# Optimization experiments

Hardware: AMD Instinct MI355X
Metric: run time of the kernel (lower is better)

The kernel has to match this reference:

```python
import jax, jax.numpy as jnp
import numpy as np

B = 4096          # events
L = 524288        # total set points (avg 128 per event)
CIN = 16          # per-point feature size (set feature 'a')
DVEC = 32         # flat feature size (feature 'b')
PHI = [128, 128, 64]
MLP = [256, 128]
EPS = 1e-5        # BatchNorm1d eps


def setup_inputs() -> dict:
    key = jax.random.key(0)
    ks = jax.random.split(key, 10)
    def n(k, shape, scale=0.05):
        return jax.random.normal(k, shape, dtype=jnp.float32) * scale
    return {
        "x_a": jax.random.normal(ks[0], (1, CIN, L), dtype=jnp.float32),
        "x_b": jax.random.normal(ks[1], (B, DVEC), dtype=jnp.float32),
        # row 0 -> counts for set feature 'a'; row 1 ignored (Reshape branch)
        "sample_indices": jnp.full((2, B), L // B, dtype=jnp.int32),
        "W1": n(ks[2], (PHI[0], CIN)),  "b1": jnp.zeros((PHI[0],), jnp.float32),
        "W2": n(ks[3], (PHI[1], PHI[0])), "b2": jnp.zeros((PHI[1],), jnp.float32),
        "W3": n(ks[4], (PHI[2], PHI[1])), "b3": jnp.zeros((PHI[2],), jnp.float32),
        "Wm1": n(ks[5], (MLP[0], PHI[2] + DVEC)), "bm1": jnp.zeros((MLP[0],), jnp.float32),
        "g1": jnp.ones((MLP[0],), jnp.float32), "be1": jnp.zeros((MLP[0],), jnp.float32),
        "Wm2": n(ks[6], (MLP[1], MLP[0])), "bm2": jnp.zeros((MLP[1],), jnp.float32),
        "g2": jnp.ones((MLP[1],), jnp.float32), "be2": jnp.zeros((MLP[1],), jnp.float32),
        "Wm3": n(ks[7], (1, MLP[1])), "bm3": jnp.zeros((1,), jnp.float32),
    }


def _bn(x, g, b):
    # BatchNorm1d, training-mode batch stats, biased variance (torch semantics)
    mu = jnp.mean(x, axis=0)
    var = jnp.var(x, axis=0)
    return (x - mu) * jax.lax.rsqrt(var + EPS) * g + b


def reference(x_a, x_b, sample_indices,
              W1, b1, W2, b2, W3, b3,
              Wm1, bm1, g1, be1, Wm2, bm2, g2, be2, Wm3, bm3):
    counts = sample_indices[0].astype(jnp.int32)                       # [B]
    bounds = jnp.concatenate([jnp.zeros((1,), jnp.int32), jnp.cumsum(counts)])  # [B+1]

    # PhiNet: pointwise Conv1d stack (kernel size 1) on [CIN, L]
    h = x_a[0]
    h = jax.nn.relu(jnp.einsum('oc,cl->ol', W1, h) + b1[:, None])
    h = jax.nn.relu(jnp.einsum('oc,cl->ol', W2, h) + b2[:, None])
    h = jax.nn.relu(jnp.einsum('oc,cl->ol', W3, h) + b3[:, None])      # [64, L]

    # fused segment-mean: point p belongs to segment j iff bounds[j] <= p < bounds[j+1]
    seg = jnp.searchsorted(bounds, jnp.arange(h.shape[1], dtype=jnp.int32), side='right') - 1
    sums = jax.ops.segment_sum(h.T, seg, num_segments=counts.shape[0])  # [B, 64]
    means = sums / jnp.maximum(counts, 1).astype(jnp.float32)[:, None]

    # feature order: sorted keys -> ('a' set repr, 'b' flat)
    z = jnp.concatenate([means, x_b.reshape(-1, DVEC)], axis=1)        # [B, 96]

    z = jax.nn.relu(_bn(z @ Wm1.T + bm1, g1, be1))
    z = jax.nn.relu(_bn(z @ Wm2.T + bm2, g2, be2))
    return jax.nn.sigmoid(z @ Wm3.T + bm3)                             # [B, 1]
```

## Files before the change

### kernel.cpp

```cpp
#include <hip/hip_runtime.h>
#include <hip/hip_bf16.h>

#define B_EVENTS 4096
#define L_PTS    524288
#define CIN      16
#define C1       128
#define C2       128
#define C3       64
#define DVEC     32
#define ZDIM     96
#define M1       256
#define M2       128
#define BN_EPS   1e-5f
#define TPTS     32
#define EPB      2

typedef __attribute__((ext_vector_type(8))) short bf16x8;
typedef __attribute__((ext_vector_type(4))) float f32x4;

__device__ __forceinline__ ushort f2bf(float x) {
    union { float f; unsigned u; } a; a.f = x;
    unsigned r = (a.u + 0x7fffu + ((a.u >> 16) & 1u)) >> 16;
    return (ushort)r;
}

__device__ __forceinline__ unsigned cvtpk(float lo, float hi) {
    unsigned r;
    asm("v_cvt_pk_bf16_f32 %0, %1, %2" : "=v"(r) : "v"(lo), "v"(hi));
    return r;
}

__device__ __forceinline__ unsigned long long pack4relu(f32x4 a) {
    union { unsigned u[2]; unsigned long long ll; } pk;
    pk.u[0] = cvtpk(fmaxf(a[0], 0.f), fmaxf(a[1], 0.f));
    pk.u[1] = cvtpk(fmaxf(a[2], 0.f), fmaxf(a[3], 0.f));
    return pk.ll;
}

__device__ __forceinline__ int ldsoff(int base, int rowSlots, int c, int sir) {
    int s = c * rowSlots + sir;
    s ^= (c & 7);
    return base + s * 16;
}

__global__ __launch_bounds__(1024) void scanprep_kernel(
    const int* __restrict__ si, int* __restrict__ bounds, float* __restrict__ stats,
    const float* __restrict__ W1, const float* __restrict__ W2, const float* __restrict__ W3,
    ushort* __restrict__ w1p, ushort* __restrict__ w2b, ushort* __restrict__ w3b)
{
    if (blockIdx.x == 0) {
        __shared__ int sh[1024];
        const int tid = threadIdx.x;
        const int c0 = si[tid*4+0], c1 = si[tid*4+1], c2 = si[tid*4+2], c3 = si[tid*4+3];
        const int s4 = c0 + c1 + c2 + c3;
        sh[tid] = s4;
        if (tid < 768) stats[tid] = 0.f;
        __syncthreads();
        for (int off = 1; off < 1024; off <<= 1) {
            int add = (tid >= off) ? sh[tid - off] : 0;
            __syncthreads();
            sh[tid] += add;
            __syncthreads();
        }
        const int excl = (tid == 0) ? 0 : sh[tid - 1];
        bounds[tid*4+0] = excl;
        bounds[tid*4+1] = excl + c0;
        bounds[tid*4+2] = excl + c0 + c1;
        bounds[tid*4+3] = excl + c0 + c1 + c2;
        if (tid == 1023) bounds[B_EVENTS] = excl + s4;
    } else {
        const int tid = (blockIdx.x - 1) * 1024 + threadIdx.x;
        const int nthr = 4 * 1024;
        for (int i = tid; i < C1 * 32; i += nthr) {
            const int r = i >> 5, k = i & 31;
            w1p[i] = (k < CIN) ? f2bf(W1[r * CIN + k]) : (ushort)0;
        }
        for (int i = tid; i < C2 * C1; i += nthr) w2b[i] = f2bf(W2[i]);
        for (int i = tid; i < C3 * C2; i += nthr) w3b[i] = f2bf(W3[i]);
    }
}

__global__ __launch_bounds__(128, 2) void phi_mfma_kernel(
    const float* __restrict__ xa, const float* __restrict__ xb,
    const int* __restrict__ bounds,
    const ushort* __restrict__ w1p, const ushort* __restrict__ w2b, const ushort* __restrict__ w3b,
    const float* __restrict__ b1, const float* __restrict__ b2, const float* __restrict__ b3,
    float* __restrict__ z)
{
    __shared__ __align__(16) char lds[18432];
    __shared__ float msum[C3];

    const int tid  = threadIdx.x;
    const int lane = tid & 63;
    const int wm   = tid >> 6;
    const int g4   = lane >> 4;
    const int c16  = lane & 15;

    bf16x8 a1[4], a2[4][4], a3[2][4];
    {
        const int r1 = wm * 64 + c16;
        #pragma unroll
        for (int mf = 0; mf < 4; ++mf)
            a1[mf] = *(const bf16x8*)&w1p[(r1 + mf * 16) * 32 + g4 * 8];
        #pragma unroll
        for (int mf = 0; mf < 4; ++mf)
            #pragma unroll
            for (int kf = 0; kf < 4; ++kf)
                a2[mf][kf] = *(const bf16x8*)&w2b[(r1 + mf * 16) * C1 + kf * 32 + g4 * 8];
        const int r3 = wm * 32 + c16;
        #pragma unroll
        for (int mf = 0; mf < 2; ++mf)
            #pragma unroll
            for (int kf = 0; kf < 4; ++kf)
                a3[mf][kf] = *(const bf16x8*)&w3b[(r3 + mf * 16) * C2 + kf * 32 + g4 * 8];
    }

    const int pt   = tid & 31;
    const int qrt  = tid >> 5;
    const int xoff = ldsoff(0, 4, pt, qrt >> 1) + (qrt & 1) * 8;

    for (int e = 0; e < EPB; ++e) {
        const int j     = blockIdx.x * EPB + e;
        const int start = bounds[j];
        const int cnt   = bounds[j + 1] - start;

        if (tid < C3) msum[tid] = 0.f;

        float xr[4];
        #pragma unroll
        for (int jj = 0; jj < 4; ++jj)
            xr[jj] = (pt < cnt) ? xa[(size_t)(qrt * 4 + jj) * L_PTS + start + pt] : 0.f;
        {
            union { unsigned u[2]; unsigned long long ll; } pk;
            pk.u[0] = cvtpk(xr[0], xr[1]);
            pk.u[1] = cvtpk(xr[2], xr[3]);
            *(unsigned long long*)(lds + xoff) = pk.ll;
        }
        __syncthreads();

        for (int p0 = 0; p0 < cnt; p0 += TPTS) {
            const bool more = (p0 + TPTS) < cnt;

            if (more) {
                const int p = p0 + TPTS + pt;
                #pragma unroll
                for (int jj = 0; jj < 4; ++jj)
                    xr[jj] = (p < cnt) ? xa[(size_t)(qrt * 4 + jj) * L_PTS + start + p] : 0.f;
            }

            {
                f32x4 acc[4][2];
                #pragma unroll
                for (int mf = 0; mf < 4; ++mf) {
                    const f32x4 bb = *(const f32x4*)&b1[wm * 64 + mf * 16 + g4 * 4];
                    acc[mf][0] = bb; acc[mf][1] = bb;
                }
                bf16x8 bfrag[2];
                #pragma unroll
                for (int nf = 0; nf < 2; ++nf)
                    bfrag[nf] = *(const bf16x8*)(lds + ldsoff(0, 4, nf * 16 + c16, g4));
                __builtin_amdgcn_s_setprio(1);
                #pragma unroll
                for (int nf = 0; nf < 2; ++nf)
                    #pragma unroll
                    for (int mf = 0; mf < 4; ++mf)
                        acc[mf][nf] = __builtin_amdgcn_mfma_f32_16x16x32_bf16(a1[mf], bfrag[nf], acc[mf][nf], 0, 0, 0);
                __builtin_amdgcn_s_setprio(0);
                #pragma unroll
                for (int mf = 0; mf < 4; ++mf)
                    #pragma unroll
                    for (int nf = 0; nf < 2; ++nf) {
                        const int c = nf * 16 + c16;
                        const int sir = (wm * 64 + mf * 16) / 8 + (g4 >> 1);
                        *(unsigned long long*)(lds + ldsoff(2048, 16, c, sir) + (g4 & 1) * 8) = pack4relu(acc[mf][nf]);
                    }
            }
            __syncthreads();

            {
                f32x4 acc[4][2];
                #pragma unroll
                for (int mf = 0; mf < 4; ++mf) {
                    const f32x4 bb = *(const f32x4*)&b2[wm * 64 + mf * 16 + g4 * 4];
                    acc[mf][0] = bb; acc[mf][1] = bb;
                }
                #pragma unroll
                for (int nf = 0; nf < 2; ++nf) {
                    const int c = nf * 16 + c16;
                    bf16x8 bk[4];
                    #pragma unroll
                    for (int kf = 0; kf < 4; ++kf)
                        bk[kf] = *(const bf16x8*)(lds + ldsoff(2048, 16, c, kf * 4 + g4));
                    __builtin_amdgcn_s_setprio(1);
                    #pragma unroll
                    for (int mf = 0; mf < 4; ++mf)
                        #pragma unroll
                        for (int kf = 0; kf < 4; ++kf)
                            acc[mf][nf] = __builtin_amdgcn_mfma_f32_16x16x32_bf16(a2[mf][kf], bk[kf], acc[mf][nf], 0, 0, 0);
                    __builtin_amdgcn_s_setprio(0);
                }
                #pragma unroll
                for (int mf = 0; mf < 4; ++mf)
                    #pragma unroll
                    for (int nf = 0; nf < 2; ++nf) {
                        const int c = nf * 16 + c16;
                        const int sir = (wm * 64 + mf * 16) / 8 + (g4 >> 1);
                        *(unsigned long long*)(lds + ldsoff(10240, 16, c, sir) + (g4 & 1) * 8) = pack4relu(acc[mf][nf]);
                    }
            }
            __syncthreads();

            if (more) {
                union { unsigned u[2]; unsigned long long ll; } pk;
                pk.u[0] = cvtpk(xr[0], xr[1]);
                pk.u[1] = cvtpk(xr[2], xr[3]);
                *(unsigned long long*)(lds + xoff) = pk.ll;
            }

            {
                f32x4 acc3[2][2];
                #pragma unroll
                for (int mf = 0; mf < 2; ++mf) {
                    const f32x4 bb = *(const f32x4*)&b3[wm * 32 + mf * 16 + g4 * 4];
                    acc3[mf][0] = bb; acc3[mf][1] = bb;
                }
                #pragma unroll
                for (int nf = 0; nf < 2; ++nf) {
                    const int c = nf * 16 + c16;
                    bf16x8 bk[4];
                    #pragma unroll
                    for (int kf = 0; kf < 4; ++kf)
                        bk[kf] = *(const bf16x8*)(lds + ldsoff(10240, 16, c, kf * 4 + g4));
                    __builtin_amdgcn_s_setprio(1);
                    #pragma unroll
                    for (int mf = 0; mf < 2; ++mf)
                        #pragma unroll
                        for (int kf = 0; kf < 4; ++kf)
                            acc3[mf][nf] = __builtin_amdgcn_mfma_f32_16x16x32_bf16(a3[mf][kf], bk[kf], acc3[mf][nf], 0, 0, 0);
                    __builtin_amdgcn_s_setprio(0);
                }
                float s[2][4];
                #pragma unroll
                for (int mf = 0; mf < 2; ++mf)
                    #pragma unroll
                    for (int r = 0; r < 4; ++r) s[mf][r] = 0.f;
                #pragma unroll
                for (int nf = 0; nf < 2; ++nf) {
                    const int col = p0 + nf * 16 + c16;
                    const bool valid = col < cnt;
                    #pragma unroll
                    for (int mf = 0; mf < 2; ++mf)
                        #pragma unroll
                        for (int r = 0; r < 4; ++r) {
                            const float v = fmaxf(acc3[mf][nf][r], 0.f);
                            if (valid) s[mf][r] += v;
                        }
                }
                #pragma unroll
                for (int mf = 0; mf < 2; ++mf)
                    #pragma unroll
                    for (int r = 0; r < 4; ++r) {
                        float v = s[mf][r];
                        #pragma unroll
                        for (int m = 1; m < 16; m <<= 1) v += __shfl_xor(v, m, 64);
                        s[mf][r] = v;
                    }
                if (c16 == 0) {
                    #pragma unroll
                    for (int mf = 0; mf < 2; ++mf)
                        #pragma unroll
                        for (int r = 0; r < 4; ++r)
                            atomicAdd(&msum[wm * 32 + mf * 16 + g4 * 4 + r], s[mf][r]);
                }
            }
            __syncthreads();
        }

        if (tid < C3) {
            const float inv = 1.f / (float)max(cnt, 1);
            z[(size_t)j * ZDIM + tid] = msum[tid] * inv;
        } else if (tid < ZDIM) {
            z[(size_t)j * ZDIM + tid] = xb[(size_t)j * DVEC + (tid - C3)];
        }
    }
}

__global__ __launch_bounds__(256) void mlp1_kernel(
    const float* __restrict__ z, const float* __restrict__ Wm1, const float* __restrict__ bm1,
    float* __restrict__ y1, float* __restrict__ gsum, float* __restrict__ gsq)
{
    __shared__ float zs[8][ZDIM + 4];
    const int r0 = blockIdx.x * 8;
    const int tid = threadIdx.x;
    for (int i = tid; i < 8 * ZDIM; i += 256) {
        const int r = i / ZDIM, c = i - r * ZDIM;
        zs[r][c] = z[(size_t)(r0 + r) * ZDIM + c];
    }
    __syncthreads();
    const int o = tid;
    float acc[8];
    const float bb = bm1[o];
    #pragma unroll
    for (int r = 0; r < 8; ++r) acc[r] = bb;
    for (int c = 0; c < ZDIM; c += 4) {
        const float4 w = *(const float4*)&Wm1[o * ZDIM + c];
        #pragma unroll
        for (int r = 0; r < 8; ++r) {
            const float4 v = *(const float4*)&zs[r][c];
            acc[r] += w.x*v.x + w.y*v.y + w.z*v.z + w.w*v.w;
        }
    }
    float s = 0.f, sq = 0.f;
    #pragma unroll
    for (int r = 0; r < 8; ++r) {
        y1[(size_t)(r0 + r) * M1 + o] = acc[r];
        s += acc[r]; sq += acc[r] * acc[r];
    }
    atomicAdd(&gsum[o], s);
    atomicAdd(&gsq[o], sq);
}

__global__ void bnfin_kernel(const float* __restrict__ gsum, const float* __restrict__ gsq,
                             const float* __restrict__ g, const float* __restrict__ be,
                             float* __restrict__ scale, float* __restrict__ shift, int n)
{
    const int o = blockIdx.x * blockDim.x + threadIdx.x;
    if (o >= n) return;
    const float mu  = gsum[o] * (1.f / B_EVENTS);
    const float var = gsq[o] * (1.f / B_EVENTS) - mu * mu;
    const float rs  = rsqrtf(var + BN_EPS);
    const float sc  = rs * g[o];
    scale[o] = sc;
    shift[o] = be[o] - mu * sc;
}

__global__ __launch_bounds__(256) void mlp2_kernel(
    const float* __restrict__ y1, const float* __restrict__ scale1, const float* __restrict__ shift1,
    const float* __restrict__ Wm2, const float* __restrict__ bm2,
    float* __restrict__ y2, float* __restrict__ gsum, float* __restrict__ gsq)
{
    __shared__ float zs[8][M1 + 4];
    const int r0 = blockIdx.x * 8;
    const int tid = threadIdx.x;
    for (int i = tid; i < 8 * M1; i += 256) {
        const int r = i >> 8, c = i & (M1 - 1);
        const float v = y1[(size_t)(r0 + r) * M1 + c];
        zs[r][c] = fmaxf(v * scale1[c] + shift1[c], 0.f);
    }
    __syncthreads();
    const int o = tid & 127;
    const int h = tid >> 7;
    float acc[4];
    const float bb = bm2[o];
    #pragma unroll
    for (int r = 0; r < 4; ++r) acc[r] = bb;
    for (int c = 0; c < M1; c += 4) {
        const float4 w = *(const float4*)&Wm2[o * M1 + c];
        #pragma unroll
        for (int r = 0; r < 4; ++r) {
            const float4 v = *(const float4*)&zs[h * 4 + r][c];
            acc[r] += w.x*v.x + w.y*v.y + w.z*v.z + w.w*v.w;
        }
    }
    float s = 0.f, sq = 0.f;
    #pragma unroll
    for (int r = 0; r < 4; ++r) {
        y2[(size_t)(r0 + h * 4 + r) * M2 + o] = acc[r];
        s += acc[r]; sq += acc[r] * acc[r];
    }
    atomicAdd(&gsum[o], s);
    atomicAdd(&gsq[o], sq);
}

__global__ __launch_bounds__(256) void final_kernel(
    const float* __restrict__ y2, const float* __restrict__ scale2, const float* __restrict__ shift2,
    const float* __restrict__ Wm3, const float* __restrict__ bm3,
    float* __restrict__ out)
{
    const int tid = threadIdx.x;
    const int w = tid >> 6, l = tid & 63;
    const int r = blockIdx.x * 4 + w;
    const float e0 = fmaxf(y2[(size_t)r * M2 + l]      * scale2[l]      + shift2[l],      0.f);
    const float e1 = fmaxf(y2[(size_t)r * M2 + 64 + l] * scale2[64 + l] + shift2[64 + l], 0.f);
    float a = e0 * Wm3[l] + e1 * Wm3[64 + l];
    #pragma unroll
    for (int off = 32; off >= 1; off >>= 1) a += __shfl_down(a, off, 64);
    if (l == 0) out[r] = 1.f / (1.f + expf(-(a + bm3[0])));
}

extern "C" void kernel_launch(void* const* d_in, const int* in_sizes, int n_in,
                              void* d_out, int out_size, void* d_ws, size_t ws_size,
                              hipStream_t stream) {
    const float* xa  = (const float*)d_in[0];
    const float* xb  = (const float*)d_in[1];
    const int*   si  = (const int*)  d_in[2];
    const float* W1  = (const float*)d_in[3];
    const float* b1  = (const float*)d_in[4];
    const float* W2  = (const float*)d_in[5];
    const float* b2  = (const float*)d_in[6];
    const float* W3  = (const float*)d_in[7];
    const float* b3  = (const float*)d_in[8];
    const float* Wm1 = (const float*)d_in[9];
    const float* bm1 = (const float*)d_in[10];
    const float* g1  = (const float*)d_in[11];
    const float* be1 = (const float*)d_in[12];
    const float* Wm2 = (const float*)d_in[13];
    const float* bm2 = (const float*)d_in[14];
    const float* g2  = (const float*)d_in[15];
    const float* be2 = (const float*)d_in[16];
    const float* Wm3 = (const float*)d_in[17];
    const float* bm3 = (const float*)d_in[18];
    float* out = (float*)d_out;

    char* ws = (char*)d_ws;
    size_t off = 0;
    auto alloc = [&](size_t bytes) -> void* {
        void* p = ws + off;
        off = (off + bytes + 255) & ~(size_t)255;
        return p;
    };
    int*    bounds = (int*)   alloc((B_EVENTS + 1) * sizeof(int));
    float*  stats  = (float*) alloc(768 * sizeof(float));
    float*  z      = (float*) alloc((size_t)B_EVENTS * ZDIM * sizeof(float));
    float*  y1     = (float*) alloc((size_t)B_EVENTS * M1 * sizeof(float));
    float*  y2     = (float*) alloc((size_t)B_EVENTS * M2 * sizeof(float));
    float*  scale1 = (float*) alloc(M1 * sizeof(float));
    float*  shift1 = (float*) alloc(M1 * sizeof(float));
    float*  scale2 = (float*) alloc(M2 * sizeof(float));
    float*  shift2 = (float*) alloc(M2 * sizeof(float));
    ushort* w1p    = (ushort*)alloc(C1 * 32 * sizeof(ushort));
    ushort* w2b    = (ushort*)alloc(C2 * C1 * sizeof(ushort));
    ushort* w3b    = (ushort*)alloc(C3 * C2 * sizeof(ushort));
    float* gsum1 = stats;
    float* gsq1  = stats + 256;
    float* gsum2 = stats + 512;
    float* gsq2  = stats + 640;

    hipLaunchKernelGGL(scanprep_kernel, dim3(5), dim3(1024), 0, stream,
                       si, bounds, stats, W1, W2, W3, w1p, w2b, w3b);
    hipLaunchKernelGGL(phi_mfma_kernel, dim3(B_EVENTS / EPB), dim3(128), 0, stream,
                       xa, xb, bounds, w1p, w2b, w3b, b1, b2, b3, z);
    hipLaunchKernelGGL(mlp1_kernel, dim3(B_EVENTS / 8), dim3(256), 0, stream,
                       z, Wm1, bm1, y1, gsum1, gsq1);
    hipLaunchKernelGGL(bnfin_kernel, dim3(1), dim3(256), 0, stream,
                       gsum1, gsq1, g1, be1, scale1, shift1, M1);
    hipLaunchKernelGGL(mlp2_kernel, dim3(B_EVENTS / 8), dim3(256), 0, stream,
                       y1, scale1, shift1, Wm2, bm2, y2, gsum2, gsq2);
    hipLaunchKernelGGL(bnfin_kernel, dim3(1), dim3(128), 0, stream,
                       gsum2, gsq2, g2, be2, scale2, shift2, M2);
    hipLaunchKernelGGL(final_kernel, dim3(B_EVENTS / 4), dim3(256), 0, stream,
                       y2, scale2, shift2, Wm3, bm3, out);
}
```

Before: 146.9 us.

## Double phi tile to 64 points with 4 waves, prefetch across events, fold BN finalize

The phi kernel now runs 256 threads over 64-point tiles, with waves split along the point dimension. It prefetches the next event's inputs during the current event's last tile, and keeps the segment sums in registers, reducing them once per event instead of using per-tile LDS atomics and a barrier. The two single-block bnfin kernels are removed, and their scale/shift computation is folded into the prologues of mlp2 and final, which cuts two launches. LDS use per block roughly doubles, which may reduce occupancy.

```diff
diff --git a/kernel.cpp b/kernel.cpp
--- a/kernel.cpp
+++ b/kernel.cpp
@@ -12,7 +12,7 @@
 #define M1       256
 #define M2       128
 #define BN_EPS   1e-5f
-#define TPTS     32
+#define TPTS     64
 #define EPB      2
 
 typedef __attribute__((ext_vector_type(8))) short bf16x8;
@@ -80,19 +80,20 @@
     }
 }
 
-__global__ __launch_bounds__(128, 2) void phi_mfma_kernel(
+__global__ __launch_bounds__(256, 2) void phi_mfma_kernel(
     const float* __restrict__ xa, const float* __restrict__ xb,
     const int* __restrict__ bounds,
     const ushort* __restrict__ w1p, const ushort* __restrict__ w2b, const ushort* __restrict__ w3b,
     const float* __restrict__ b1, const float* __restrict__ b2, const float* __restrict__ b3,
     float* __restrict__ z)
 {
-    __shared__ __align__(16) char lds[18432];
-    __shared__ float msum[C3];
+    __shared__ __align__(16) char lds[37376];
 
     const int tid  = threadIdx.x;
     const int lane = tid & 63;
-    const int wm   = tid >> 6;
+    const int wid  = tid >> 6;
+    const int wm   = wid >> 1;
+    const int wn   = wid & 1;
     const int g4   = lane >> 4;
     const int c16  = lane & 15;
 
@@ -115,37 +116,54 @@
                 a3[mf][kf] = *(const bf16x8*)&w3b[(r3 + mf * 16) * C2 + kf * 32 + g4 * 8];
     }
 
-    const int pt   = tid & 31;
-    const int qrt  = tid >> 5;
-    const int xoff = ldsoff(0, 4, pt, qrt >> 1) + (qrt & 1) * 8;
-
-    for (int e = 0; e < EPB; ++e) {
-        const int j     = blockIdx.x * EPB + e;
-        const int start = bounds[j];
-        const int cnt   = bounds[j + 1] - start;
-
-        if (tid < C3) msum[tid] = 0.f;
-
-        float xr[4];
-        #pragma unroll
-        for (int jj = 0; jj < 4; ++jj)
-            xr[jj] = (pt < cnt) ? xa[(size_t)(qrt * 4 + jj) * L_PTS + start + pt] : 0.f;
-        {
+    const int pt = tid & 63;
+    const int q  = tid >> 6;
+    const int xw = pt * 32 + q * 8;
+
+    if (tid < 128)
+        *(unsigned long long*)(lds + (tid >> 1) * 32 + 16 + (tid & 1) * 8) = 0ull;
+
+    int j     = blockIdx.x * EPB;
+    int start = bounds[j];
+    int end   = bounds[j + 1];
+    int cnt   = end - start;
+    bool staged = false;
+
+    for (int e = 0; e < EPB; ++e, ++j) {
+        int end2 = 0, cnt2 = 0;
+        if (e + 1 < EPB) { end2 = bounds[j + 2]; cnt2 = end2 - end; }
+
+        if (!staged) {
             union { unsigned u[2]; unsigned long long ll; } pk;
-            pk.u[0] = cvtpk(xr[0], xr[1]);
-            pk.u[1] = cvtpk(xr[2], xr[3]);
-            *(unsigned long long*)(lds + xoff) = pk.ll;
-        }
-        __syncthreads();
+            float v0 = (pt < cnt) ? xa[(size_t)(q * 4 + 0) * L_PTS + start + pt] : 0.f;
+            float v1 = (pt < cnt) ? xa[(size_t)(q * 4 + 1) * L_PTS + start + pt] : 0.f;
+            float v2 = (pt < cnt) ? xa[(size_t)(q * 4 + 2) * L_PTS + start + pt] : 0.f;
+            float v3 = (pt < cnt) ? xa[(size_t)(q * 4 + 3) * L_PTS + start + pt] : 0.f;
+            pk.u[0] = cvtpk(v0, v1);
+            pk.u[1] = cvtpk(v2, v3);
+            *(unsigned long long*)(lds + xw) = pk.ll;
+            __syncthreads();
+        }
+
+        float s[2][4];
+        #pragma unroll
+        for (int mf = 0; mf < 2; ++mf)
+            #pragma unroll
+            for (int r = 0; r < 4; ++r) s[mf][r] = 0.f;
 
         for (int p0 = 0; p0 < cnt; p0 += TPTS) {
-            const bool more = (p0 + TPTS) < cnt;
-
-            if (more) {
-                const int p = p0 + TPTS + pt;
-                #pragma unroll
-                for (int jj = 0; jj < 4; ++jj)
-                    xr[jj] = (p < cnt) ? xa[(size_t)(qrt * 4 + jj) * L_PTS + start + p] : 0.f;
+            const bool inEvt  = (p0 + TPTS) < cnt;
+            const bool nxtEvt = !inEvt && (e + 1 < EPB);
+            const bool pre    = inEvt || nxtEvt;
+
+            float xr0 = 0.f, xr1 = 0.f, xr2 = 0.f, xr3 = 0.f;
+            if (pre) {
+                const int nbase = inEvt ? (start + p0 + TPTS) : end;
+                const int nrem  = inEvt ? (cnt - p0 - TPTS) : cnt2;
+                xr0 = (pt < nrem) ? xa[(size_t)(q * 4 + 0) * L_PTS + nbase + pt] : 0.f;
+                xr1 = (pt < nrem) ? xa[(size_t)(q * 4 + 1) * L_PTS + nbase + pt] : 0.f;
+                xr2 = (pt < nrem) ? xa[(size_t)(q * 4 + 2) * L_PTS + nbase + pt] : 0.f;
+                xr3 = (pt < nrem) ? xa[(size_t)(q * 4 + 3) * L_PTS + nbase + pt] : 0.f;
             }
 
             {
@@ -158,7 +176,7 @@
                 bf16x8 bfrag[2];
                 #pragma unroll
                 for (int nf = 0; nf < 2; ++nf)
-                    bfrag[nf] = *(const bf16x8*)(lds + ldsoff(0, 4, nf * 16 + c16, g4));
+                    bfrag[nf] = *(const bf16x8*)(lds + (wn * 32 + nf * 16 + c16) * 32 + g4 * 16);
                 __builtin_amdgcn_s_setprio(1);
                 #pragma unroll
                 for (int nf = 0; nf < 2; ++nf)
@@ -170,9 +188,9 @@
                 for (int mf = 0; mf < 4; ++mf)
                     #pragma unroll
                     for (int nf = 0; nf < 2; ++nf) {
-                        const int c = nf * 16 + c16;
+                        const int c = wn * 32 + nf * 16 + c16;
                         const int sir = (wm * 64 + mf * 16) / 8 + (g4 >> 1);
-                        *(unsigned long long*)(lds + ldsoff(2048, 16, c, sir) + (g4 & 1) * 8) = pack4relu(acc[mf][nf]);
+                        *(unsigned long long*)(lds + ldsoff(4096, 16, c, sir) + (g4 & 1) * 8) = pack4relu(acc[mf][nf]);
                     }
             }
             __syncthreads();
@@ -186,11 +204,11 @@
                 }
                 #pragma unroll
                 for (int nf = 0; nf < 2; ++nf) {
-                    const int c = nf * 16 + c16;
+                    const int c = wn * 32 + nf * 16 + c16;
                     bf16x8 bk[4];
                     #pragma unroll
                     for (int kf = 0; kf < 4; ++kf)
-                        bk[kf] = *(const bf16x8*)(lds + ldsoff(2048, 16, c, kf * 4 + g4));
+                        bk[kf] = *(const bf16x8*)(lds + ldsoff(4096, 16, c, kf * 4 + g4));
                     __builtin_amdgcn_s_setprio(1);
                     #pragma unroll
                     for (int mf = 0; mf < 4; ++mf)
@@ -199,23 +217,22 @@
                             acc[mf][nf] = __builtin_amdgcn_mfma_f32_16x16x32_bf16(a2[mf][kf], bk[kf], acc[mf][nf], 0, 0, 0);
                     __builtin_amdgcn_s_setprio(0);
                 }
+                if (pre) {
+                    union { unsigned u[2]; unsigned long long ll; } pk;
+                    pk.u[0] = cvtpk(xr0, xr1);
+                    pk.u[1] = cvtpk(xr2, xr3);
+                    *(unsigned long long*)(lds + xw) = pk.ll;
+                }
                 #pragma unroll
                 for (int mf = 0; mf < 4; ++mf)
                     #pragma unroll
                     for (int nf = 0; nf < 2; ++nf) {
-                        const int c = nf * 16 + c16;
+                        const int c = wn * 32 + nf * 16 + c16;
                         const int sir = (wm * 64 + mf * 16) / 8 + (g4 >> 1);
-                        *(unsigned long long*)(lds + ldsoff(10240, 16, c, sir) + (g4 & 1) * 8) = pack4relu(acc[mf][nf]);
+                        *(unsigned long long*)(lds + ldsoff(20480, 16, c, sir) + (g4 & 1) * 8) = pack4relu(acc[mf][nf]);
                     }
             }
             __syncthreads();
-
-            if (more) {
-                union { unsigned u[2]; unsigned long long ll; } pk;
-                pk.u[0] = cvtpk(xr[0], xr[1]);
-                pk.u[1] = cvtpk(xr[2], xr[3]);
-                *(unsigned long long*)(lds + xoff) = pk.ll;
-            }
 
             {
                 f32x4 acc3[2][2];
@@ -226,11 +243,11 @@
                 }
                 #pragma unroll
                 for (int nf = 0; nf < 2; ++nf) {
-                    const int c = nf * 16 + c16;
+                    const int c = wn * 32 + nf * 16 + c16;
                     bf16x8 bk[4];
                     #pragma unroll
                     for (int kf = 0; kf < 4; ++kf)
-                        bk[kf] = *(const bf16x8*)(lds + ldsoff(10240, 16, c, kf * 4 + g4));
+                        bk[kf] = *(const bf16x8*)(lds + ldsoff(20480, 16, c, kf * 4 + g4));
                     __builtin_amdgcn_s_setprio(1);
                     #pragma unroll
                     for (int mf = 0; mf < 2; ++mf)
@@ -239,14 +256,9 @@
                             acc3[mf][nf] = __builtin_amdgcn_mfma_f32_16x16x32_bf16(a3[mf][kf], bk[kf], acc3[mf][nf], 0, 0, 0);
                     __builtin_amdgcn_s_setprio(0);
                 }
-                float s[2][4];
-                #pragma unroll
-                for (int mf = 0; mf < 2; ++mf)
-                    #pragma unroll
-                    for (int r = 0; r < 4; ++r) s[mf][r] = 0.f;
                 #pragma unroll
                 for (int nf = 0; nf < 2; ++nf) {
-                    const int col = p0 + nf * 16 + c16;
+                    const int col = p0 + wn * 32 + nf * 16 + c16;
                     const bool valid = col < cnt;
                     #pragma unroll
                     for (int mf = 0; mf < 2; ++mf)
@@ -256,32 +268,35 @@
                             if (valid) s[mf][r] += v;
                         }
                 }
-                #pragma unroll
-                for (int mf = 0; mf < 2; ++mf)
-                    #pragma unroll
-                    for (int r = 0; r < 4; ++r) {
-                        float v = s[mf][r];
-                        #pragma unroll
-                        for (int m = 1; m < 16; m <<= 1) v += __shfl_xor(v, m, 64);
-                        s[mf][r] = v;
-                    }
-                if (c16 == 0) {
-                    #pragma unroll
-                    for (int mf = 0; mf < 2; ++mf)
-                        #pragma unroll
-                        for (int r = 0; r < 4; ++r)
-                            atomicAdd(&msum[wm * 32 + mf * 16 + g4 * 4 + r], s[mf][r]);
-                }
-            }
-            __syncthreads();
-        }
-
-        if (tid < C3) {
+            }
+        }
+
+        #pragma unroll
+        for (int mf = 0; mf < 2; ++mf)
+            #pragma unroll
+            for (int r = 0; r < 4; ++r) {
+                float v = s[mf][r];
+                v += __shfl_xor(v, 1, 64);
+                v += __shfl_xor(v, 2, 64);
+                v += __shfl_xor(v, 4, 64);
+                v += __shfl_xor(v, 8, 64);
+                if (c16 == 0)
+                    *(float*)(lds + 36864 + (wn * 64 + wm * 32 + mf * 16 + g4 * 4 + r) * 4) = v;
+            }
+        __syncthreads();
+        {
             const float inv = 1.f / (float)max(cnt, 1);
-            z[(size_t)j * ZDIM + tid] = msum[tid] * inv;
-        } else if (tid < ZDIM) {
-            z[(size_t)j * ZDIM + tid] = xb[(size_t)j * DVEC + (tid - C3)];
-        }
+            if (tid < C3) {
+                const float v = *(const float*)(lds + 36864 + tid * 4)
+                              + *(const float*)(lds + 36864 + 256 + tid * 4);
+                z[(size_t)j * ZDIM + tid] = v * inv;
+            } else if (tid < ZDIM) {
+                z[(size_t)j * ZDIM + tid] = xb[(size_t)j * DVEC + (tid - C3)];
+            }
+        }
+
+        staged = (cnt > 0) && (e + 1 < EPB);
+        if (e + 1 < EPB) { start = end; cnt = cnt2; end = end2; }
     }
 }
 
@@ -320,32 +335,29 @@
     atomicAdd(&gsq[o], sq);
 }
 
-__global__ void bnfin_kernel(const float* __restrict__ gsum, const float* __restrict__ gsq,
-                             const float* __restrict__ g, const float* __restrict__ be,
-                             float* __restrict__ scale, float* __restrict__ shift, int n)
-{
-    const int o = blockIdx.x * blockDim.x + threadIdx.x;
-    if (o >= n) return;
-    const float mu  = gsum[o] * (1.f / B_EVENTS);
-    const float var = gsq[o] * (1.f / B_EVENTS) - mu * mu;
-    const float rs  = rsqrtf(var + BN_EPS);
-    const float sc  = rs * g[o];
-    scale[o] = sc;
-    shift[o] = be[o] - mu * sc;
-}
-
 __global__ __launch_bounds__(256) void mlp2_kernel(
-    const float* __restrict__ y1, const float* __restrict__ scale1, const float* __restrict__ shift1,
+    const float* __restrict__ y1,
+    const float* __restrict__ gsum1, const float* __restrict__ gsq1,
+    const float* __restrict__ g1, const float* __restrict__ be1,
     const float* __restrict__ Wm2, const float* __restrict__ bm2,
     float* __restrict__ y2, float* __restrict__ gsum, float* __restrict__ gsq)
 {
     __shared__ float zs[8][M1 + 4];
+    __shared__ float sc[M1], sh[M1];
     const int r0 = blockIdx.x * 8;
     const int tid = threadIdx.x;
+    {
+        const float mu  = gsum1[tid] * (1.f / B_EVENTS);
+        const float var = gsq1[tid] * (1.f / B_EVENTS) - mu * mu;
+        const float s0  = rsqrtf(var + BN_EPS) * g1[tid];
+        sc[tid] = s0;
+        sh[tid] = be1[tid] - mu * s0;
+    }
+    __syncthreads();
     for (int i = tid; i < 8 * M1; i += 256) {
         const int r = i >> 8, c = i & (M1 - 1);
         const float v = y1[(size_t)(r0 + r) * M1 + c];
-        zs[r][c] = fmaxf(v * scale1[c] + shift1[c], 0.f);
+        zs[r][c] = fmaxf(v * sc[c] + sh[c], 0.f);
     }
     __syncthreads();
     const int o = tid & 127;
@@ -373,15 +385,26 @@
 }
 
 __global__ __launch_bounds__(256) void final_kernel(
-    const float* __restrict__ y2, const float* __restrict__ scale2, const float* __restrict__ shift2,
+    const float* __restrict__ y2,
+    const float* __restrict__ gsum2, const float* __restrict__ gsq2,
+    const float* __restrict__ g2, const float* __restrict__ be2,
     const float* __restrict__ Wm3, const float* __restrict__ bm3,
     float* __restrict__ out)
 {
+    __shared__ float sc[M2], sh[M2];
     const int tid = threadIdx.x;
+    if (tid < M2) {
+        const float mu  = gsum2[tid] * (1.f / B_EVENTS);
+        const float var = gsq2[tid] * (1.f / B_EVENTS) - mu * mu;
+        const float s0  = rsqrtf(var + BN_EPS) * g2[tid];
+        sc[tid] = s0;
+        sh[tid] = be2[tid] - mu * s0;
+    }
+    __syncthreads();
     const int w = tid >> 6, l = tid & 63;
     const int r = blockIdx.x * 4 + w;
-    const float e0 = fmaxf(y2[(size_t)r * M2 + l]      * scale2[l]      + shift2[l],      0.f);
-    const float e1 = fmaxf(y2[(size_t)r * M2 + 64 + l] * scale2[64 + l] + shift2[64 + l], 0.f);
+    const float e0 = fmaxf(y2[(size_t)r * M2 + l]      * sc[l]      + sh[l],      0.f);
+    const float e1 = fmaxf(y2[(size_t)r * M2 + 64 + l] * sc[64 + l] + sh[64 + l], 0.f);
     float a = e0 * Wm3[l] + e1 * Wm3[64 + l];
     #pragma unroll
     for (int off = 32; off >= 1; off >>= 1) a += __shfl_down(a, off, 64);
@@ -424,10 +447,6 @@
     float*  z      = (float*) alloc((size_t)B_EVENTS * ZDIM * sizeof(float));
     float*  y1     = (float*) alloc((size_t)B_EVENTS * M1 * sizeof(float));
     float*  y2     = (float*) alloc((size_t)B_EVENTS * M2 * sizeof(float));
-    float*  scale1 = (float*) alloc(M1 * sizeof(float));
-    float*  shift1 = (float*) alloc(M1 * sizeof(float));
-    float*  scale2 = (float*) alloc(M2 * sizeof(float));
-    float*  shift2 = (float*) alloc(M2 * sizeof(float));
     ushort* w1p    = (ushort*)alloc(C1 * 32 * sizeof(ushort));
     ushort* w2b    = (ushort*)alloc(C2 * C1 * sizeof(ushort));
     ushort* w3b    = (ushort*)alloc(C3 * C2 * sizeof(ushort));
@@ -438,16 +457,12 @@
 
     hipLaunchKernelGGL(scanprep_kernel, dim3(5), dim3(1024), 0, stream,
                        si, bounds, stats, W1, W2, W3, w1p, w2b, w3b);
-    hipLaunchKernelGGL(phi_mfma_kernel, dim3(B_EVENTS / EPB), dim3(128), 0, stream,
+    hipLaunchKernelGGL(phi_mfma_kernel, dim3(B_EVENTS / EPB), dim3(256), 0, stream,
                        xa, xb, bounds, w1p, w2b, w3b, b1, b2, b3, z);
     hipLaunchKernelGGL(mlp1_kernel, dim3(B_EVENTS / 8), dim3(256), 0, stream,
                        z, Wm1, bm1, y1, gsum1, gsq1);
-    hipLaunchKernelGGL(bnfin_kernel, dim3(1), dim3(256), 0, stream,
-                       gsum1, gsq1, g1, be1, scale1, shift1, M1);
     hipLaunchKernelGGL(mlp2_kernel, dim3(B_EVENTS / 8), dim3(256), 0, stream,
-                       y1, scale1, shift1, Wm2, bm2, y2, gsum2, gsq2);
-    hipLaunchKernelGGL(bnfin_kernel, dim3(1), dim3(128), 0, stream,
-                       gsum2, gsq2, g2, be2, scale2, shift2, M2);
+                       y1, gsum1, gsq1, g1, be1, Wm2, bm2, y2, gsum2, gsq2);
     hipLaunchKernelGGL(final_kernel, dim3(B_EVENTS / 4), dim3(256), 0, stream,
-                       y2, scale2, shift2, Wm3, bm3, out);
-}
+                       y2, gsum2, gsq2, g2, be2, Wm3, bm3, out);
+}
```

Result: faster. 143.4 us (-2.3%).
